# Kernel optimization log

Hardware: AMD Instinct MI355X
Metric: run time of the kernel (lower is better)

## Reference

```python
import jax, jax.numpy as jnp
import numpy as np

B, NQ, NK, D, H, DR, MLPD = 32, 32, 4096, 256, 8, 2, 2048
ID = D // DR  # internal dim for downsampled cross-attention
EPS = 1e-5


def _ln(x, g, b):
    m = jnp.mean(x, -1, keepdims=True)
    v = jnp.mean((x - m) ** 2, -1, keepdims=True)
    return (x - m) / jnp.sqrt(v + EPS) * g + b


def _attn(q, k, v, qw, qb, kw, kb, vw, vb, ow, ob):
    # linear projections (weights stored as [in, out])
    q = q @ qw + qb
    k = k @ kw + kb
    v = v @ vw + vb
    b, nq, c = q.shape
    d = c // H
    qh = q.reshape(b, nq, H, d)
    kh = k.reshape(b, -1, H, d)
    vh = v.reshape(b, -1, H, d)
    scores = jnp.einsum('bqhd,bkhd->bhqk', qh, kh) * (1.0 / np.sqrt(d))
    a = jax.nn.softmax(scores, axis=-1)
    o = jnp.einsum('bhqk,bkhd->bqhd', a, vh).reshape(b, nq, c)
    return o @ ow + ob


def _forward(queries, keys, query_pe,
             sa_qw, sa_qb, sa_kw, sa_kb, sa_vw, sa_vb, sa_ow, sa_ob,
             t2i_qw, t2i_qb, t2i_kw, t2i_kb, t2i_vw, t2i_vb, t2i_ow, t2i_ob,
             i2t_qw, i2t_qb, i2t_kw, i2t_kb, i2t_vw, i2t_vb, i2t_ow, i2t_ob,
             mlp_w1, mlp_b1, mlp_w2, mlp_b2,
             ln1_g, ln1_b, ln2_g, ln2_b, ln3_g, ln3_b, ln4_g, ln4_b):
    # skip_first_layer_pe = False
    queries = queries + query_pe
    attn_out = _attn(queries, queries, queries,
                     sa_qw, sa_qb, sa_kw, sa_kb, sa_vw, sa_vb, sa_ow, sa_ob)
    queries = _ln(queries + attn_out, ln1_g, ln1_b)
    # cross attention: tokens -> image
    q = queries + query_pe
    attn_out = _attn(q, keys, keys,
                     t2i_qw, t2i_qb, t2i_kw, t2i_kb, t2i_vw, t2i_vb, t2i_ow, t2i_ob)
    queries = _ln(queries + attn_out, ln2_g, ln2_b)
    # MLP block (num_layers=1): act(x W1 + b1) W2 + b2, act = ReLU
    mlp_out = jax.nn.relu(queries @ mlp_w1 + mlp_b1) @ mlp_w2 + mlp_b2
    queries = _ln(queries + mlp_out, ln3_g, ln3_b)
    # cross attention: image -> tokens
    q = queries + query_pe
    attn_out = _attn(keys, q, queries,
                     i2t_qw, i2t_qb, i2t_kw, i2t_kb, i2t_vw, i2t_vb, i2t_ow, i2t_ob)
    keys = _ln(keys + attn_out, ln4_g, ln4_b)
    return queries, keys


def setup_inputs() -> dict:
    key = jax.random.key(0)
    ks = iter(jax.random.split(key, 64))
    def w(shape, s=0.02):
        return jax.random.normal(next(ks), shape, jnp.float32) * s
    inp = {
        'queries': w((B, NQ, D), 1.0),
        'keys': w((B, NK, D), 1.0),
        'query_pe': w((B, NQ, D), 1.0),
    }
    for pre, idim in [('sa', D), ('t2i', ID), ('i2t', ID)]:
        inp[pre + '_qw'] = w((D, idim)); inp[pre + '_qb'] = jnp.zeros((idim,), jnp.float32)
        inp[pre + '_kw'] = w((D, idim)); inp[pre + '_kb'] = jnp.zeros((idim,), jnp.float32)
        inp[pre + '_vw'] = w((D, idim)); inp[pre + '_vb'] = jnp.zeros((idim,), jnp.float32)
        inp[pre + '_ow'] = w((idim, D)); inp[pre + '_ob'] = jnp.zeros((D,), jnp.float32)
    inp['mlp_w1'] = w((D, MLPD)); inp['mlp_b1'] = jnp.zeros((MLPD,), jnp.float32)
    inp['mlp_w2'] = w((MLPD, D)); inp['mlp_b2'] = jnp.zeros((D,), jnp.float32)
    for i in range(1, 5):
        inp['ln%d_g' % i] = jnp.ones((D,), jnp.float32)
        inp['ln%d_b' % i] = jnp.zeros((D,), jnp.float32)
    return inp


def reference(queries, keys, query_pe,
              sa_qw, sa_qb, sa_kw, sa_kb, sa_vw, sa_vb, sa_ow, sa_ob,
              t2i_qw, t2i_qb, t2i_kw, t2i_kb, t2i_vw, t2i_vb, t2i_ow, t2i_ob,
              i2t_qw, i2t_qb, i2t_kw, i2t_kb, i2t_vw, i2t_vb, i2t_ow, i2t_ob,
              mlp_w1, mlp_b1, mlp_w2, mlp_b2,
              ln1_g, ln1_b, ln2_g, ln2_b, ln3_g, ln3_b, ln4_g, ln4_b):
    return _forward(queries, keys, query_pe,
                    sa_qw, sa_qb, sa_kw, sa_kb, sa_vw, sa_vb, sa_ow, sa_ob,
                    t2i_qw, t2i_qb, t2i_kw, t2i_kb, t2i_vw, t2i_vb, t2i_ow, t2i_ob,
                    i2t_qw, i2t_qb, i2t_kw, i2t_kb, i2t_vw, i2t_vb, i2t_ow, i2t_ob,
                    mlp_w1, mlp_b1, mlp_w2, mlp_b2,
                    ln1_g, ln1_b, ln2_g, ln2_b, ln3_g, ln3_b, ln4_g, ln4_b)
```

## Files before the change

kernel.cpp:

```cpp
#include <hip/hip_runtime.h>

typedef unsigned short u16;
typedef __attribute__((ext_vector_type(8))) short s16x8;
typedef __attribute__((ext_vector_type(4))) float f32x4;
typedef __attribute__((ext_vector_type(8))) unsigned short u16x8;

__device__ __forceinline__ float b2f(u16 u) {
  union { unsigned int i; float f; } v; v.i = ((unsigned int)u) << 16; return v.f;
}
__device__ __forceinline__ u16 f2b(float f) {
  union { float f; unsigned int i; } v; v.f = f;
  unsigned int r = v.i + 0x7FFFu + ((v.i >> 16) & 1u);
  return (u16)(r >> 16);
}
__device__ __forceinline__ int pk2(float a, float b) {
  return (int)f2b(a) | ((int)f2b(b) << 16);
}

template<bool RELU>
__global__ void __launch_bounds__(256) k_gemm(
    const u16* __restrict__ A, const u16* __restrict__ Wt,
    const float* __restrict__ bias, u16* __restrict__ C, int N, int K)
{
  __shared__ int4 smem4[2048];
  char* AsB = (char*)smem4;
  char* WsB = (char*)smem4 + 16384;
  const int t = threadIdx.x;
  const int lane = t & 63, wid = t >> 6;
  const int wm = wid >> 1, wn = wid & 1;
  const int l16 = lane & 15, lhi = lane >> 4;
  const int bCol = blockIdx.x * 128;
  const int bRow = blockIdx.y * 128;

  f32x4 acc[4][4];
#pragma unroll
  for (int i = 0; i < 4; ++i)
#pragma unroll
    for (int j = 0; j < 4; ++j) acc[i][j] = (f32x4){0.f, 0.f, 0.f, 0.f};

  int4 av[4], wv[4];
  auto LOADT = [&](int kt) {
    const int k0 = kt << 6;
#pragma unroll
    for (int i = 0; i < 4; ++i) {
      int L = i * 4096 + t * 16;
      int r = L >> 7, cl = (L >> 4) & 7;
      av[i] = *(const int4*)(A + (size_t)(bRow + r) * K + k0 + cl * 8);
      wv[i] = *(const int4*)(Wt + (size_t)(bCol + r) * K + k0 + cl * 8);
    }
  };
  const int nk = K >> 6;
  LOADT(0);
  for (int kt = 0; kt < nk; ++kt) {
    if (kt) __syncthreads();
#pragma unroll
    for (int i = 0; i < 4; ++i) {
      int L = i * 4096 + t * 16;
      int r = L >> 7, cl = (L >> 4) & 7;
      int off = r * 128 + ((cl ^ (r & 7)) << 4);
      *(int4*)(AsB + off) = av[i];
      *(int4*)(WsB + off) = wv[i];
    }
    __syncthreads();
    if (kt + 1 < nk) LOADT(kt + 1);
#pragma unroll
    for (int kk = 0; kk < 2; ++kk) {
      s16x8 af[4], bfr[4];
#pragma unroll
      for (int mt = 0; mt < 4; ++mt) {
        int r = wm * 64 + mt * 16 + l16;
        int ch = kk * 4 + lhi;
        af[mt] = *(const s16x8*)(AsB + r * 128 + ((ch ^ (r & 7)) << 4));
      }
#pragma unroll
      for (int nt = 0; nt < 4; ++nt) {
        int r = wn * 64 + nt * 16 + l16;
        int ch = kk * 4 + lhi;
        bfr[nt] = *(const s16x8*)(WsB + r * 128 + ((ch ^ (r & 7)) << 4));
      }
#pragma unroll
      for (int mt = 0; mt < 4; ++mt)
#pragma unroll
        for (int nt = 0; nt < 4; ++nt)
          acc[mt][nt] = __builtin_amdgcn_mfma_f32_16x16x32_bf16(
              af[mt], bfr[nt], acc[mt][nt], 0, 0, 0);
    }
  }
#pragma unroll
  for (int mt = 0; mt < 4; ++mt) {
#pragma unroll
    for (int nt = 0; nt < 4; ++nt) {
      int cg = bCol + wn * 64 + nt * 16 + l16;
      float bv = bias[cg];
#pragma unroll
      for (int rg = 0; rg < 4; ++rg) {
        int rgl = bRow + wm * 64 + mt * 16 + lhi * 4 + rg;
        float v = acc[mt][nt][rg] + bv;
        if (RELU) v = fmaxf(v, 0.f);
        C[(size_t)rgl * N + cg] = f2b(v);
      }
    }
  }
}

__global__ void __launch_bounds__(512, 2) k_gemm_kvq(
    const float* __restrict__ A, const u16* __restrict__ Wt,
    const float* __restrict__ bias, u16* __restrict__ KV, u16* __restrict__ QB)
{
  __shared__ char smem[65536];
  char* AsB = smem;
  char* WsB = smem + 16384;
  const int t = threadIdx.x;
  const int lane = t & 63, wid = t >> 6;
  const int wm = wid >> 2, wn = wid & 3;
  const int l16 = lane & 15, lhi = lane >> 4;
  const int bRow = blockIdx.x * 128;

  f32x4 acc[4][6];
#pragma unroll
  for (int i = 0; i < 4; ++i)
#pragma unroll
    for (int j = 0; j < 6; ++j) acc[i][j] = (f32x4){0.f, 0.f, 0.f, 0.f};

  float4 a0r[2], a1r[2];
  int4 wv[6];
  auto LOADT = [&](int kt) {
    const int k0 = kt << 6;
#pragma unroll
    for (int i = 0; i < 2; ++i) {
      int L = i * 8192 + t * 16;
      int r = L >> 7, cl = (L >> 4) & 7;
      const float* Af = A + (size_t)(bRow + r) * 256 + k0 + cl * 8;
      a0r[i] = *(const float4*)Af;
      a1r[i] = *(const float4*)(Af + 4);
    }
#pragma unroll
    for (int i = 0; i < 6; ++i) {
      int L = i * 8192 + t * 16;
      int r = L >> 7, cl = (L >> 4) & 7;
      wv[i] = *(const int4*)(Wt + (size_t)r * 256 + k0 + cl * 8);
    }
  };
  LOADT(0);
  for (int kt = 0; kt < 4; ++kt) {
    if (kt) __syncthreads();
#pragma unroll
    for (int i = 0; i < 2; ++i) {
      int L = i * 8192 + t * 16;
      int r = L >> 7, cl = (L >> 4) & 7;
      int4 p = (int4){pk2(a0r[i].x, a0r[i].y), pk2(a0r[i].z, a0r[i].w),
                      pk2(a1r[i].x, a1r[i].y), pk2(a1r[i].z, a1r[i].w)};
      *(int4*)(AsB + r * 128 + ((cl ^ (r & 7)) << 4)) = p;
    }
#pragma unroll
    for (int i = 0; i < 6; ++i) {
      int L = i * 8192 + t * 16;
      int r = L >> 7, cl = (L >> 4) & 7;
      *(int4*)(WsB + r * 128 + ((cl ^ (r & 7)) << 4)) = wv[i];
    }
    __syncthreads();
    if (kt < 3) LOADT(kt + 1);
#pragma unroll
    for (int kk = 0; kk < 2; ++kk) {
      s16x8 af[4], bfr[6];
#pragma unroll
      for (int mt = 0; mt < 4; ++mt) {
        int r = wm * 64 + mt * 16 + l16;
        int ch = kk * 4 + lhi;
        af[mt] = *(const s16x8*)(AsB + r * 128 + ((ch ^ (r & 7)) << 4));
      }
#pragma unroll
      for (int nt = 0; nt < 6; ++nt) {
        int r = wn * 96 + nt * 16 + l16;
        int ch = kk * 4 + lhi;
        bfr[nt] = *(const s16x8*)(WsB + r * 128 + ((ch ^ (r & 7)) << 4));
      }
#pragma unroll
      for (int mt = 0; mt < 4; ++mt)
#pragma unroll
        for (int nt = 0; nt < 6; ++nt)
          acc[mt][nt] = __builtin_amdgcn_mfma_f32_16x16x32_bf16(
              af[mt], bfr[nt], acc[mt][nt], 0, 0, 0);
    }
  }
  u16* ldsO = (u16*)smem;
  for (int half = 0; half < 2; ++half) {
    __syncthreads();
    if (wm == half) {
#pragma unroll
      for (int mt = 0; mt < 4; ++mt) {
#pragma unroll
        for (int nt = 0; nt < 6; ++nt) {
          int cg = wn * 96 + nt * 16 + l16;
          float bv = bias[cg];
#pragma unroll
          for (int rg = 0; rg < 4; ++rg) {
            int r = mt * 16 + lhi * 4 + rg;
            ldsO[r * 384 + cg] = f2b(acc[mt][nt][rg] + bv);
          }
        }
      }
    }
    __syncthreads();
#pragma unroll
    for (int i = 0; i < 6; ++i) {
      int chunk = i * 512 + t;
      int r = chunk / 48, c8 = chunk - r * 48;
      int row = bRow + half * 64 + r;
      int4 v = *(int4*)(ldsO + r * 384 + c8 * 8);
      if (c8 < 32) *(int4*)(KV + (size_t)row * 256 + c8 * 8) = v;
      else         *(int4*)(QB + (size_t)row * 128 + (c8 - 32) * 8) = v;
    }
  }
}

__global__ void __launch_bounds__(256) k_gemm_ln(
    const u16* __restrict__ A, const u16* __restrict__ Wt,
    const float* __restrict__ bias, const float* __restrict__ res,
    const float* __restrict__ g, const float* __restrict__ bl,
    float* __restrict__ out)
{
  __shared__ int4 smem4[2560];
  __shared__ float rsum[2][32][2], rsq[2][32][2];
  char* AsB = (char*)smem4;
  char* WsB = (char*)smem4 + 8192;
  const int t = threadIdx.x;
  const int lane = t & 63, wid = t >> 6;
  const int wm = wid >> 1, wn = wid & 1;
  const int l16 = lane & 15, lhi = lane >> 4;
  const int bRow = blockIdx.x * 64;

  f32x4 acc[2][8];
#pragma unroll
  for (int i = 0; i < 2; ++i)
#pragma unroll
    for (int j = 0; j < 8; ++j) acc[i][j] = (f32x4){0.f, 0.f, 0.f, 0.f};

  int4 av[2], wv[8];
  auto LOADT = [&](int kt) {
    const int k0 = kt << 6;
#pragma unroll
    for (int i = 0; i < 2; ++i) {
      int L = i * 4096 + t * 16;
      int r = L >> 7, cl = (L >> 4) & 7;
      av[i] = *(const int4*)(A + (size_t)(bRow + r) * 128 + k0 + cl * 8);
    }
#pragma unroll
    for (int i = 0; i < 8; ++i) {
      int L = i * 4096 + t * 16;
      int r = L >> 7, cl = (L >> 4) & 7;
      wv[i] = *(const int4*)(Wt + (size_t)r * 128 + k0 + cl * 8);
    }
  };
  LOADT(0);
  for (int kt = 0; kt < 2; ++kt) {
    if (kt) __syncthreads();
#pragma unroll
    for (int i = 0; i < 2; ++i) {
      int L = i * 4096 + t * 16;
      int r = L >> 7, cl = (L >> 4) & 7;
      *(int4*)(AsB + r * 128 + ((cl ^ (r & 7)) << 4)) = av[i];
    }
#pragma unroll
    for (int i = 0; i < 8; ++i) {
      int L = i * 4096 + t * 16;
      int r = L >> 7, cl = (L >> 4) & 7;
      *(int4*)(WsB + r * 128 + ((cl ^ (r & 7)) << 4)) = wv[i];
    }
    __syncthreads();
    if (kt == 0) LOADT(1);
#pragma unroll
    for (int kk = 0; kk < 2; ++kk) {
      s16x8 af[2], bfr[8];
#pragma unroll
      for (int mt = 0; mt < 2; ++mt) {
        int r = wm * 32 + mt * 16 + l16;
        int ch = kk * 4 + lhi;
        af[mt] = *(const s16x8*)(AsB + r * 128 + ((ch ^ (r & 7)) << 4));
      }
#pragma unroll
      for (int nt = 0; nt < 8; ++nt) {
        int r = wn * 128 + nt * 16 + l16;
        int ch = kk * 4 + lhi;
        bfr[nt] = *(const s16x8*)(WsB + r * 128 + ((ch ^ (r & 7)) << 4));
      }
#pragma unroll
      for (int mt = 0; mt < 2; ++mt)
#pragma unroll
        for (int nt = 0; nt < 8; ++nt)
          acc[mt][nt] = __builtin_amdgcn_mfma_f32_16x16x32_bf16(
              af[mt], bfr[nt], acc[mt][nt], 0, 0, 0);
    }
  }
#pragma unroll
  for (int mt = 0; mt < 2; ++mt) {
#pragma unroll
    for (int nt = 0; nt < 8; ++nt) {
      int cg = wn * 128 + nt * 16 + l16;
      float bv = bias[cg];
#pragma unroll
      for (int rg = 0; rg < 4; ++rg) {
        int row = bRow + wm * 32 + mt * 16 + lhi * 4 + rg;
        acc[mt][nt][rg] += bv + res[(size_t)row * 256 + cg];
      }
    }
  }
#pragma unroll
  for (int mt = 0; mt < 2; ++mt) {
#pragma unroll
    for (int rg = 0; rg < 4; ++rg) {
      float ps = 0.f, pq = 0.f;
#pragma unroll
      for (int nt = 0; nt < 8; ++nt) {
        float v = acc[mt][nt][rg];
        ps += v; pq += v * v;
      }
#pragma unroll
      for (int msk = 1; msk < 16; msk <<= 1) {
        ps += __shfl_xor(ps, msk);
        pq += __shfl_xor(pq, msk);
      }
      if (l16 == 0) {
        int rl = mt * 16 + lhi * 4 + rg;
        rsum[wm][rl][wn] = ps;
        rsq[wm][rl][wn] = pq;
      }
    }
  }
  __syncthreads();
#pragma unroll
  for (int mt = 0; mt < 2; ++mt) {
#pragma unroll
    for (int rg = 0; rg < 4; ++rg) {
      int rl = mt * 16 + lhi * 4 + rg;
      float ts = rsum[wm][rl][0] + rsum[wm][rl][1];
      float tq = rsq[wm][rl][0] + rsq[wm][rl][1];
      float mean = ts * (1.f / 256.f);
      float var = tq * (1.f / 256.f) - mean * mean;
      float rstd = rsqrtf(var + 1e-5f);
      int row = bRow + wm * 32 + rl;
#pragma unroll
      for (int nt = 0; nt < 8; ++nt) {
        int cg = wn * 128 + nt * 16 + l16;
        out[(size_t)row * 256 + cg] =
            (acc[mt][nt][rg] - mean) * rstd * g[cg] + bl[cg];
      }
    }
  }
}

struct TDesc { const float* src; void* dst; int K; int N; int mode; int blk0; };
struct TArgs { TDesc d[24]; int n; };

__global__ void __launch_bounds__(256) k_trans(TArgs a)
{
  int blk = blockIdx.x;
  int i = 0;
  while (i + 1 < a.n && blk >= a.d[i + 1].blk0) ++i;
  TDesc td = a.d[i];
  int e = (blk - td.blk0) * 256 + threadIdx.x;
  int tot = td.K * td.N;
  if (e >= tot) return;
  if (td.mode == 0) {
    int k = e / td.N, n = e - k * td.N;
    ((u16*)td.dst)[(size_t)n * td.K + k] = f2b(td.src[e]);
  } else {
    ((float*)td.dst)[e] = td.src[e];
  }
}

__global__ void __launch_bounds__(256) k_addpe(
    const float* __restrict__ q, const float* __restrict__ pe,
    float* __restrict__ outf, u16* __restrict__ outb)
{
  int i = blockIdx.x * 256 + threadIdx.x;
  float v = q[i] + pe[i];
  outf[i] = v;
  outb[i] = f2b(v);
}

__global__ void __launch_bounds__(64) k_attn_sa(
    const u16* __restrict__ QKV, u16* __restrict__ out)
{
  __shared__ float Q[32][33], K[32][33], V[32][33];
  int b = blockIdx.x >> 3, h = blockIdx.x & 7;
  int t = threadIdx.x;
  for (int idx = t; idx < 1024; idx += 64) {
    int i = idx >> 5, d = idx & 31;
    size_t base = (size_t)(b * 32 + i) * 768 + h * 32 + d;
    Q[i][d] = b2f(QKV[base]);
    K[i][d] = b2f(QKV[base + 256]);
    V[i][d] = b2f(QKV[base + 512]);
  }
  __syncthreads();
  int i = t & 31, half = t >> 5;
  float s[16];
#pragma unroll
  for (int jj = 0; jj < 16; ++jj) {
    int j = half * 16 + jj;
    float a = 0.f;
#pragma unroll
    for (int d = 0; d < 32; ++d) a += Q[i][d] * K[j][d];
    s[jj] = a * 0.17677669529663687f;
  }
  float m = s[0];
#pragma unroll
  for (int jj = 1; jj < 16; ++jj) m = fmaxf(m, s[jj]);
  m = fmaxf(m, __shfl_xor(m, 32));
  float sum = 0.f;
#pragma unroll
  for (int jj = 0; jj < 16; ++jj) { s[jj] = __expf(s[jj] - m); sum += s[jj]; }
  sum += __shfl_xor(sum, 32);
  float o[32];
#pragma unroll
  for (int d = 0; d < 32; ++d) o[d] = 0.f;
#pragma unroll
  for (int jj = 0; jj < 16; ++jj) {
    int j = half * 16 + jj;
    float p = s[jj];
#pragma unroll
    for (int d = 0; d < 32; ++d) o[d] += p * V[j][d];
  }
  float inv = 1.f / sum;
#pragma unroll
  for (int d = 0; d < 32; ++d) {
    float v = o[d] + __shfl_xor(o[d], 32);
    if (half == 0) out[(size_t)(b * 32 + i) * 256 + h * 32 + d] = f2b(v * inv);
  }
}

__global__ void __launch_bounds__(128) k_attn_t2i_part(
    const u16* __restrict__ Qt, const u16* __restrict__ KV,
    float* __restrict__ part)
{
  __shared__ int4 kvs[4096];
  int c = blockIdx.x, b = blockIdx.y;
  int tid = threadIdx.x;
  const int4* src = (const int4*)(KV + ((size_t)b * 4096 + c * 128) * 256);
  for (int i = tid; i < 4096; i += 128) kvs[i] = src[i];
  __syncthreads();
  int qp = tid >> 3, h = tid & 7;
  const u16* lds = (const u16*)kvs;

  float q0[16], q1[16];
  {
    const u16* p0 = Qt + (size_t)(b * 32 + qp) * 128 + h * 16;
    const u16* p1 = Qt + (size_t)(b * 32 + qp + 16) * 128 + h * 16;
    u16x8 a0 = *(const u16x8*)p0, b0 = *(const u16x8*)(p0 + 8);
    u16x8 a1 = *(const u16x8*)p1, b1 = *(const u16x8*)(p1 + 8);
#pragma unroll
    for (int e = 0; e < 8; ++e) {
      q0[e] = b2f(a0[e]); q0[8 + e] = b2f(b0[e]);
      q1[e] = b2f(a1[e]); q1[8 + e] = b2f(b1[e]);
    }
  }
  float m0 = -INFINITY, s0 = 0.f, m1 = -INFINITY, s1 = 0.f;
  float acc0[16], acc1[16];
#pragma unroll
  for (int d = 0; d < 16; ++d) { acc0[d] = 0.f; acc1[d] = 0.f; }

  for (int j = 0; j < 128; ++j) {
    const u16* kr = lds + j * 256 + h * 16;
    u16x8 ka = *(const u16x8*)kr;
    u16x8 kb = *(const u16x8*)(kr + 8);
    float l0 = 0.f, l1 = 0.f;
#pragma unroll
    for (int e = 0; e < 8; ++e) {
      float klo = b2f(ka[e]), khi = b2f(kb[e]);
      l0 += q0[e] * klo + q0[8 + e] * khi;
      l1 += q1[e] * klo + q1[8 + e] * khi;
    }
    l0 *= 0.25f; l1 *= 0.25f;
    const u16* vr = kr + 128;
    u16x8 va = *(const u16x8*)vr;
    u16x8 vb = *(const u16x8*)(vr + 8);
    float nm0 = fmaxf(m0, l0), nm1 = fmaxf(m1, l1);
    float c0 = __expf(m0 - nm0), p0 = __expf(l0 - nm0);
    float c1 = __expf(m1 - nm1), p1 = __expf(l1 - nm1);
    s0 = s0 * c0 + p0; s1 = s1 * c1 + p1;
#pragma unroll
    for (int e = 0; e < 8; ++e) {
      float vlo = b2f(va[e]), vhi = b2f(vb[e]);
      acc0[e] = acc0[e] * c0 + p0 * vlo;
      acc0[8 + e] = acc0[8 + e] * c0 + p0 * vhi;
      acc1[e] = acc1[e] * c1 + p1 * vlo;
      acc1[8 + e] = acc1[8 + e] * c1 + p1 * vhi;
    }
    m0 = nm0; m1 = nm1;
  }
  float* r0 = part + (((size_t)(b * 32 + qp) * 8 + h) * 32 + c) * 18;
  float* r1 = part + (((size_t)(b * 32 + qp + 16) * 8 + h) * 32 + c) * 18;
#pragma unroll
  for (int d = 0; d < 16; ++d) { r0[d] = acc0[d]; r1[d] = acc1[d]; }
  r0[16] = m0; r0[17] = s0;
  r1[16] = m1; r1[17] = s1;
}

__global__ void __launch_bounds__(256) k_attn_t2i_merge(
    const float* __restrict__ part, u16* __restrict__ out)
{
  int b = blockIdx.x >> 3, h = blockIdx.x & 7;
  int q = threadIdx.x >> 3, ds = threadIdx.x & 7;
  const float* base = part + (((size_t)(b * 32 + q) * 8 + h) * 32) * 18;
  float mg = -INFINITY;
#pragma unroll 4
  for (int c = 0; c < 32; ++c) mg = fmaxf(mg, base[c * 18 + 16]);
  float sg = 0.f, a0 = 0.f, a1 = 0.f;
#pragma unroll 4
  for (int c = 0; c < 32; ++c) {
    const float* rec = base + c * 18;
    float w = __expf(rec[16] - mg);
    sg += rec[17] * w;
    a0 += rec[ds * 2] * w;
    a1 += rec[ds * 2 + 1] * w;
  }
  float inv = 1.f / sg;
  u16* op = out + (size_t)(b * 32 + q) * 128 + h * 16 + ds * 2;
  op[0] = f2b(a0 * inv);
  op[1] = f2b(a1 * inv);
}

__global__ void __launch_bounds__(256) k_attn_i2t(
    const u16* __restrict__ Qb, const u16* __restrict__ Kc,
    const u16* __restrict__ Vc, u16* __restrict__ out)
{
  __shared__ float Kl[32][132], Vl[32][132];
  int blk = blockIdx.x;
  int b = blk >> 7;
  int r0 = (blk & 127) * 32;
  for (int idx = threadIdx.x; idx < 4096; idx += 256) {
    int j = idx >> 7, c = idx & 127;
    Kl[j][c] = b2f(Kc[(size_t)(b * 32 + j) * 128 + c]);
    Vl[j][c] = b2f(Vc[(size_t)(b * 32 + j) * 128 + c]);
  }
  __syncthreads();
  int lr = threadIdx.x >> 3, h = threadIdx.x & 7;
  size_t row = (size_t)b * 4096 + r0 + lr;
  const u16* qp = Qb + row * 128 + h * 16;
  float q[16];
  {
    u16x8 qa = *(const u16x8*)qp;
    u16x8 qb2 = *(const u16x8*)(qp + 8);
#pragma unroll
    for (int e = 0; e < 8; ++e) { q[e] = b2f(qa[e]); q[8 + e] = b2f(qb2[e]); }
  }
  float lg[32];
  float mx = -INFINITY;
#pragma unroll
  for (int j = 0; j < 32; ++j) {
    float a = 0.f;
#pragma unroll
    for (int d = 0; d < 16; ++d) a += q[d] * Kl[j][h * 16 + d];
    lg[j] = a * 0.25f;
    mx = fmaxf(mx, lg[j]);
  }
  float sum = 0.f;
#pragma unroll
  for (int j = 0; j < 32; ++j) { lg[j] = __expf(lg[j] - mx); sum += lg[j]; }
  float acc[16];
#pragma unroll
  for (int d = 0; d < 16; ++d) acc[d] = 0.f;
#pragma unroll
  for (int j = 0; j < 32; ++j) {
    float p = lg[j];
#pragma unroll
    for (int d = 0; d < 16; ++d) acc[d] += p * Vl[j][h * 16 + d];
  }
  float inv = 1.f / sum;
  u16* op = out + row * 128 + h * 16;
#pragma unroll
  for (int d = 0; d < 16; ++d) op[d] = f2b(acc[d] * inv);
}

__global__ void __launch_bounds__(256) k_addln_small(
    const float* __restrict__ res, const u16* __restrict__ delta,
    const float* __restrict__ g, const float* __restrict__ bb,
    float* outf, u16* outb, const float* pe, u16* outpe)
{
  int row = blockIdx.x * 4 + (threadIdx.x >> 6);
  int lane = threadIdx.x & 63;
  size_t base = (size_t)row * 256 + lane * 4;
  float4 xv = *(const float4*)(res + base);
  ushort4 dv = *(const ushort4*)(delta + base);
  float v0 = xv.x + b2f(dv.x), v1 = xv.y + b2f(dv.y);
  float v2 = xv.z + b2f(dv.z), v3 = xv.w + b2f(dv.w);
  float sum = v0 + v1 + v2 + v3;
  float sq = v0 * v0 + v1 * v1 + v2 * v2 + v3 * v3;
#pragma unroll
  for (int msk = 1; msk < 64; msk <<= 1) {
    sum += __shfl_xor(sum, msk);
    sq += __shfl_xor(sq, msk);
  }
  float mean = sum * (1.f / 256.f);
  float var = sq * (1.f / 256.f) - mean * mean;
  float rstd = rsqrtf(var + 1e-5f);
  float4 gv = *(const float4*)(g + lane * 4);
  float4 bv = *(const float4*)(bb + lane * 4);
  float y0 = (v0 - mean) * rstd * gv.x + bv.x;
  float y1 = (v1 - mean) * rstd * gv.y + bv.y;
  float y2 = (v2 - mean) * rstd * gv.z + bv.z;
  float y3 = (v3 - mean) * rstd * gv.w + bv.w;
  if (outf) { float4 o{y0, y1, y2, y3}; *(float4*)(outf + base) = o; }
  if (outb) {
    ushort4 o{f2b(y0), f2b(y1), f2b(y2), f2b(y3)};
    *(ushort4*)(outb + base) = o;
  }
  if (outpe) {
    float4 pv = *(const float4*)(pe + base);
    ushort4 o{f2b(y0 + pv.x), f2b(y1 + pv.y), f2b(y2 + pv.z), f2b(y3 + pv.w)};
    *(ushort4*)(outpe + base) = o;
  }
}

extern "C" void kernel_launch(void* const* d_in, const int* in_sizes, int n_in,
                              void* d_out, int out_size, void* d_ws, size_t ws_size,
                              hipStream_t stream)
{
  (void)in_sizes; (void)n_in; (void)out_size; (void)ws_size;
  const float* queries = (const float*)d_in[0];
  const float* keys    = (const float*)d_in[1];
  const float* qpe     = (const float*)d_in[2];
  const float* sa_qw = (const float*)d_in[3];  const float* sa_qb = (const float*)d_in[4];
  const float* sa_kw = (const float*)d_in[5];  const float* sa_kb = (const float*)d_in[6];
  const float* sa_vw = (const float*)d_in[7];  const float* sa_vb = (const float*)d_in[8];
  const float* sa_ow = (const float*)d_in[9];  const float* sa_ob = (const float*)d_in[10];
  const float* t2i_qw = (const float*)d_in[11]; const float* t2i_qb = (const float*)d_in[12];
  const float* t2i_kw = (const float*)d_in[13]; const float* t2i_kb = (const float*)d_in[14];
  const float* t2i_vw = (const float*)d_in[15]; const float* t2i_vb = (const float*)d_in[16];
  const float* t2i_ow = (const float*)d_in[17]; const float* t2i_ob = (const float*)d_in[18];
  const float* i2t_qw = (const float*)d_in[19]; const float* i2t_qb = (const float*)d_in[20];
  const float* i2t_kw = (const float*)d_in[21]; const float* i2t_kb = (const float*)d_in[22];
  const float* i2t_vw = (const float*)d_in[23]; const float* i2t_vb = (const float*)d_in[24];
  const float* i2t_ow = (const float*)d_in[25]; const float* i2t_ob = (const float*)d_in[26];
  const float* mlp_w1 = (const float*)d_in[27]; const float* mlp_b1 = (const float*)d_in[28];
  const float* mlp_w2 = (const float*)d_in[29]; const float* mlp_b2 = (const float*)d_in[30];
  const float* ln1_g = (const float*)d_in[31]; const float* ln1_b = (const float*)d_in[32];
  const float* ln2_g = (const float*)d_in[33]; const float* ln2_b = (const float*)d_in[34];
  const float* ln3_g = (const float*)d_in[35]; const float* ln3_b = (const float*)d_in[36];
  const float* ln4_g = (const float*)d_in[37]; const float* ln4_b = (const float*)d_in[38];

  float* out_q = (float*)d_out;
  float* out_k = out_q + 262144;

  u16* kvbuf  = (u16*)out_k;
  u16* qb_big = (u16*)out_k + 33554432;
  float* t2i_part = (float*)((u16*)out_k + 50331648);

  char* ws = (char*)d_ws;
  size_t off = 0;
  auto alloc = [&](size_t bytes) -> char* {
    char* p = ws + off;
    off += (bytes + 255) & ~(size_t)255;
    return p;
  };
  u16* wt_saqkv = (u16*)alloc(768 * 256 * 2);
  u16* wt_saow  = (u16*)alloc(256 * 256 * 2);
  u16* wt_t2iq  = (u16*)alloc(128 * 256 * 2);
  u16* wt_kvq   = (u16*)alloc(384 * 256 * 2);
  u16* wt_t2io  = (u16*)alloc(256 * 128 * 2);
  u16* wt_i2tk  = (u16*)alloc(128 * 256 * 2);
  u16* wt_i2tv  = (u16*)alloc(128 * 256 * 2);
  u16* wt_i2to  = (u16*)alloc(256 * 128 * 2);
  u16* wt_w1    = (u16*)alloc(2048 * 256 * 2);
  u16* wt_w2    = (u16*)alloc(256 * 2048 * 2);
  float* b_saqkv = (float*)alloc(768 * 4);
  float* b_kvq   = (float*)alloc(384 * 4);
  float* q0f = (float*)alloc(262144 * 4);
  float* q1f = (float*)alloc(262144 * 4);
  float* q2f = (float*)alloc(262144 * 4);
  u16* q0b   = (u16*)alloc(262144 * 2);
  u16* qkvs  = (u16*)alloc(786432 * 2);
  u16* attn1 = (u16*)alloc(262144 * 2);
  u16* o1    = (u16*)alloc(262144 * 2);
  u16* q1pe  = (u16*)alloc(262144 * 2);
  u16* qt    = (u16*)alloc(131072 * 2);
  u16* at2   = (u16*)alloc(131072 * 2);
  u16* o2    = (u16*)alloc(262144 * 2);
  u16* q2b   = (u16*)alloc(262144 * 2);
  u16* hbuf  = (u16*)alloc(2097152 * 2);
  u16* mo    = (u16*)alloc(262144 * 2);
  u16* q3b   = (u16*)alloc(262144 * 2);
  u16* q3pe  = (u16*)alloc(262144 * 2);
  u16* kc    = (u16*)alloc(131072 * 2);
  u16* vc    = (u16*)alloc(131072 * 2);
  u16* ab_big = (u16*)alloc((size_t)16777216 * 2);

  TArgs ta{};
  int nb = 0, id = 0;
  auto addT = [&](const float* s, void* d, int K, int N, int mode) {
    ta.d[id].src = s; ta.d[id].dst = d; ta.d[id].K = K; ta.d[id].N = N;
    ta.d[id].mode = mode; ta.d[id].blk0 = nb;
    nb += (K * N + 255) / 256;
    ++id;
  };
  addT(sa_qw, wt_saqkv, 256, 256, 0);
  addT(sa_kw, wt_saqkv + 256 * 256, 256, 256, 0);
  addT(sa_vw, wt_saqkv + 512 * 256, 256, 256, 0);
  addT(sa_ow, wt_saow, 256, 256, 0);
  addT(t2i_qw, wt_t2iq, 256, 128, 0);
  addT(t2i_kw, wt_kvq, 256, 128, 0);
  addT(t2i_vw, wt_kvq + 128 * 256, 256, 128, 0);
  addT(i2t_qw, wt_kvq + 256 * 256, 256, 128, 0);
  addT(t2i_ow, wt_t2io, 128, 256, 0);
  addT(i2t_kw, wt_i2tk, 256, 128, 0);
  addT(i2t_vw, wt_i2tv, 256, 128, 0);
  addT(i2t_ow, wt_i2to, 128, 256, 0);
  addT(mlp_w1, wt_w1, 256, 2048, 0);
  addT(mlp_w2, wt_w2, 2048, 256, 0);
  addT(sa_qb, b_saqkv, 1, 256, 1);
  addT(sa_kb, b_saqkv + 256, 1, 256, 1);
  addT(sa_vb, b_saqkv + 512, 1, 256, 1);
  addT(t2i_kb, b_kvq, 1, 128, 1);
  addT(t2i_vb, b_kvq + 128, 1, 128, 1);
  addT(i2t_qb, b_kvq + 256, 1, 128, 1);
  ta.n = id;
  k_trans<<<nb, 256, 0, stream>>>(ta);

  k_addpe<<<1024, 256, 0, stream>>>(queries, qpe, q0f, q0b);
  k_gemm<false><<<dim3(6, 8), 256, 0, stream>>>(q0b, wt_saqkv, b_saqkv,
                                                qkvs, 768, 256);
  k_attn_sa<<<256, 64, 0, stream>>>(qkvs, attn1);
  k_gemm<false><<<dim3(2, 8), 256, 0, stream>>>(attn1, wt_saow, sa_ob,
                                                o1, 256, 256);
  k_addln_small<<<256, 256, 0, stream>>>(q0f, o1, ln1_g, ln1_b, q1f, nullptr,
                                         qpe, q1pe);
  k_gemm<false><<<dim3(1, 8), 256, 0, stream>>>(q1pe, wt_t2iq, t2i_qb,
                                                qt, 128, 256);
  k_gemm_kvq<<<1024, 512, 0, stream>>>(keys, wt_kvq, b_kvq, kvbuf, qb_big);
  k_attn_t2i_part<<<dim3(32, 32), 128, 0, stream>>>(qt, kvbuf, t2i_part);
  k_attn_t2i_merge<<<256, 256, 0, stream>>>(t2i_part, at2);
  k_gemm<false><<<dim3(2, 8), 256, 0, stream>>>(at2, wt_t2io, t2i_ob,
                                                o2, 256, 128);
  k_addln_small<<<256, 256, 0, stream>>>(q1f, o2, ln2_g, ln2_b, q2f, q2b,
                                         nullptr, nullptr);
  k_gemm<true><<<dim3(16, 8), 256, 0, stream>>>(q2b, wt_w1, mlp_b1,
                                                hbuf, 2048, 256);
  k_gemm<false><<<dim3(2, 8), 256, 0, stream>>>(hbuf, wt_w2, mlp_b2,
                                                mo, 256, 2048);
  k_addln_small<<<256, 256, 0, stream>>>(q2f, mo, ln3_g, ln3_b, out_q, q3b,
                                         qpe, q3pe);
  k_gemm<false><<<dim3(1, 8), 256, 0, stream>>>(q3pe, wt_i2tk, i2t_kb,
                                                kc, 128, 256);
  k_gemm<false><<<dim3(1, 8), 256, 0, stream>>>(q3b, wt_i2tv, i2t_vb,
                                                vc, 128, 256);
  k_attn_i2t<<<4096, 256, 0, stream>>>(qb_big, kc, vc, ab_big);
  k_gemm_ln<<<2048, 256, 0, stream>>>(ab_big, wt_i2to, i2t_ob, keys,
                                      ln4_g, ln4_b, out_k);
}
```

Measured before the change: 609.0 us.

## Fuse t2i attention into KVQ projection and GEMM+LayerNorm for query path

The key/value/query projection kernel now keeps the projected K/V tile in shared memory and runs the token-to-image partial attention directly from it. This removes the round trip of the large KV buffer through global memory and one kernel launch. Separately, the three small output-projection GEMMs are fused with residual-add plus LayerNorm into a new k_gemm_lnq kernel, dropping intermediate buffers and launches. The trade-offs are that the fused kernel uses more LDS (80KB), which may lower occupancy, only half its threads do the attention tail, and the LN GEMMs run on just 16 blocks.

After: 642.3 us. 1.05x slower.

```diff
diff --git a/kernel.cpp b/kernel.cpp
--- a/kernel.cpp
+++ b/kernel.cpp
@@ -103,11 +103,12 @@
   }
 }
 
-__global__ void __launch_bounds__(512, 2) k_gemm_kvq(
+__global__ void __launch_bounds__(512, 2) k_kvq_t2i(
     const float* __restrict__ A, const u16* __restrict__ Wt,
-    const float* __restrict__ bias, u16* __restrict__ KV, u16* __restrict__ QB)
-{
-  __shared__ char smem[65536];
+    const float* __restrict__ bias, const u16* __restrict__ Qt,
+    u16* __restrict__ QB, float* __restrict__ part)
+{
+  __shared__ char smem[81920];
   char* AsB = smem;
   char* WsB = smem + 16384;
   const int t = threadIdx.x;
@@ -183,7 +184,8 @@
               af[mt], bfr[nt], acc[mt][nt], 0, 0, 0);
     }
   }
-  u16* ldsO = (u16*)smem;
+  u16* ldsKV = (u16*)smem;
+  u16* ldsQB = (u16*)(smem + 65536);
   for (int half = 0; half < 2; ++half) {
     __syncthreads();
     if (wm == half) {
@@ -196,20 +198,200 @@
 #pragma unroll
           for (int rg = 0; rg < 4; ++rg) {
             int r = mt * 16 + lhi * 4 + rg;
-            ldsO[r * 384 + cg] = f2b(acc[mt][nt][rg] + bv);
+            u16 o = f2b(acc[mt][nt][rg] + bv);
+            if (cg < 256) ldsKV[(half * 64 + r) * 256 + cg] = o;
+            else          ldsQB[r * 128 + (cg - 256)] = o;
           }
         }
       }
     }
     __syncthreads();
 #pragma unroll
-    for (int i = 0; i < 6; ++i) {
+    for (int i = 0; i < 2; ++i) {
       int chunk = i * 512 + t;
-      int r = chunk / 48, c8 = chunk - r * 48;
-      int row = bRow + half * 64 + r;
-      int4 v = *(int4*)(ldsO + r * 384 + c8 * 8);
-      if (c8 < 32) *(int4*)(KV + (size_t)row * 256 + c8 * 8) = v;
-      else         *(int4*)(QB + (size_t)row * 128 + (c8 - 32) * 8) = v;
+      int r = chunk >> 4, c8 = chunk & 15;
+      *(int4*)(QB + (size_t)(bRow + half * 64 + r) * 128 + c8 * 8) =
+          *(int4*)(ldsQB + r * 128 + c8 * 8);
+    }
+  }
+  if (t < 256) {
+    int q = t >> 3, h = t & 7;
+    int b = bRow >> 12, c = (bRow >> 7) & 31;
+    float q16[16];
+    {
+      const u16* qp = Qt + (size_t)(b * 32 + q) * 128 + h * 16;
+      u16x8 qa = *(const u16x8*)qp;
+      u16x8 qb = *(const u16x8*)(qp + 8);
+#pragma unroll
+      for (int e = 0; e < 8; ++e) { q16[e] = b2f(qa[e]); q16[8 + e] = b2f(qb[e]); }
+    }
+    float m = -INFINITY, s = 0.f, a16[16];
+#pragma unroll
+    for (int d = 0; d < 16; ++d) a16[d] = 0.f;
+    for (int j = 0; j < 128; ++j) {
+      const u16* kr = ldsKV + j * 256 + h * 16;
+      u16x8 ka = *(const u16x8*)kr;
+      u16x8 kb = *(const u16x8*)(kr + 8);
+      float lg = 0.f;
+#pragma unroll
+      for (int e = 0; e < 8; ++e) lg += q16[e] * b2f(ka[e]) + q16[8 + e] * b2f(kb[e]);
+      lg *= 0.25f;
+      const u16* vr = ldsKV + j * 256 + 128 + h * 16;
+      u16x8 va = *(const u16x8*)vr;
+      u16x8 vb = *(const u16x8*)(vr + 8);
+      float nm = fmaxf(m, lg);
+      float corr = __expf(m - nm), p = __expf(lg - nm);
+      s = s * corr + p;
+#pragma unroll
+      for (int e = 0; e < 8; ++e) {
+        a16[e] = a16[e] * corr + p * b2f(va[e]);
+        a16[8 + e] = a16[8 + e] * corr + p * b2f(vb[e]);
+      }
+      m = nm;
+    }
+    float* rec = part + (((size_t)(b * 32 + q) * 8 + h) * 32 + c) * 18;
+#pragma unroll
+    for (int d = 0; d < 16; ++d) rec[d] = a16[d];
+    rec[16] = m; rec[17] = s;
+  }
+}
+
+__global__ void __launch_bounds__(256) k_gemm_lnq(
+    const u16* __restrict__ A, const u16* __restrict__ Wt,
+    const float* __restrict__ bias, const float* __restrict__ res,
+    const float* __restrict__ g, const float* __restrict__ bl,
+    const float* __restrict__ pe,
+    float* outf, u16* outb, u16* outpe, int K)
+{
+  __shared__ int4 smem4[2560];
+  __shared__ float rsum[2][32][2], rsq[2][32][2];
+  char* AsB = (char*)smem4;
+  char* WsB = (char*)smem4 + 8192;
+  const int t = threadIdx.x;
+  const int lane = t & 63, wid = t >> 6;
+  const int wm = wid >> 1, wn = wid & 1;
+  const int l16 = lane & 15, lhi = lane >> 4;
+  const int bRow = blockIdx.x * 64;
+
+  f32x4 acc[2][8];
+#pragma unroll
+  for (int i = 0; i < 2; ++i)
+#pragma unroll
+    for (int j = 0; j < 8; ++j) acc[i][j] = (f32x4){0.f, 0.f, 0.f, 0.f};
+
+  int4 av[2], wv[8];
+  auto LOADT = [&](int kt) {
+    const int k0 = kt << 6;
+#pragma unroll
+    for (int i = 0; i < 2; ++i) {
+      int L = i * 4096 + t * 16;
+      int r = L >> 7, cl = (L >> 4) & 7;
+      av[i] = *(const int4*)(A + (size_t)(bRow + r) * K + k0 + cl * 8);
+    }
+#pragma unroll
+    for (int i = 0; i < 8; ++i) {
+      int L = i * 4096 + t * 16;
+      int r = L >> 7, cl = (L >> 4) & 7;
+      wv[i] = *(const int4*)(Wt + (size_t)r * K + k0 + cl * 8);
+    }
+  };
+  const int nk = K >> 6;
+  LOADT(0);
+  for (int kt = 0; kt < nk; ++kt) {
+    if (kt) __syncthreads();
+#pragma unroll
+    for (int i = 0; i < 2; ++i) {
+      int L = i * 4096 + t * 16;
+      int r = L >> 7, cl = (L >> 4) & 7;
+      *(int4*)(AsB + r * 128 + ((cl ^ (r & 7)) << 4)) = av[i];
+    }
+#pragma unroll
+    for (int i = 0; i < 8; ++i) {
+      int L = i * 4096 + t * 16;
+      int r = L >> 7, cl = (L >> 4) & 7;
+      *(int4*)(WsB + r * 128 + ((cl ^ (r & 7)) << 4)) = wv[i];
+    }
+    __syncthreads();
+    if (kt + 1 < nk) LOADT(kt + 1);
+#pragma unroll
+    for (int kk = 0; kk < 2; ++kk) {
+      s16x8 af[2], bfr[8];
+#pragma unroll
+      for (int mt = 0; mt < 2; ++mt) {
+        int r = wm * 32 + mt * 16 + l16;
+        int ch = kk * 4 + lhi;
+        af[mt] = *(const s16x8*)(AsB + r * 128 + ((ch ^ (r & 7)) << 4));
+      }
+#pragma unroll
+      for (int nt = 0; nt < 8; ++nt) {
+        int r = wn * 128 + nt * 16 + l16;
+        int ch = kk * 4 + lhi;
+        bfr[nt] = *(const s16x8*)(WsB + r * 128 + ((ch ^ (r & 7)) << 4));
+      }
+#pragma unroll
+      for (int mt = 0; mt < 2; ++mt)
+#pragma unroll
+        for (int nt = 0; nt < 8; ++nt)
+          acc[mt][nt] = __builtin_amdgcn_mfma_f32_16x16x32_bf16(
+              af[mt], bfr[nt], acc[mt][nt], 0, 0, 0);
+    }
+  }
+#pragma unroll
+  for (int mt = 0; mt < 2; ++mt) {
+#pragma unroll
+    for (int nt = 0; nt < 8; ++nt) {
+      int cg = wn * 128 + nt * 16 + l16;
+      float bv = bias[cg];
+#pragma unroll
+      for (int rg = 0; rg < 4; ++rg) {
+        int row = bRow + wm * 32 + mt * 16 + lhi * 4 + rg;
+        acc[mt][nt][rg] += bv + res[(size_t)row * 256 + cg];
+      }
+    }
+  }
+#pragma unroll
+  for (int mt = 0; mt < 2; ++mt) {
+#pragma unroll
+    for (int rg = 0; rg < 4; ++rg) {
+      float ps = 0.f, pq = 0.f;
+#pragma unroll
+      for (int nt = 0; nt < 8; ++nt) {
+        float v = acc[mt][nt][rg];
+        ps += v; pq += v * v;
+      }
+#pragma unroll
+      for (int msk = 1; msk < 16; msk <<= 1) {
+        ps += __shfl_xor(ps, msk);
+        pq += __shfl_xor(pq, msk);
+      }
+      if (l16 == 0) {
+        int rl = mt * 16 + lhi * 4 + rg;
+        rsum[wm][rl][wn] = ps;
+        rsq[wm][rl][wn] = pq;
+      }
+    }
+  }
+  __syncthreads();
+#pragma unroll
+  for (int mt = 0; mt < 2; ++mt) {
+#pragma unroll
+    for (int rg = 0; rg < 4; ++rg) {
+      int rl = mt * 16 + lhi * 4 + rg;
+      float ts = rsum[wm][rl][0] + rsum[wm][rl][1];
+      float tq = rsq[wm][rl][0] + rsq[wm][rl][1];
+      float mean = ts * (1.f / 256.f);
+      float var = tq * (1.f / 256.f) - mean * mean;
+      float rstd = rsqrtf(var + 1e-5f);
+      int row = bRow + wm * 32 + rl;
+#pragma unroll
+      for (int nt = 0; nt < 8; ++nt) {
+        int cg = wn * 128 + nt * 16 + l16;
+        size_t idx = (size_t)row * 256 + cg;
+        float y = (acc[mt][nt][rg] - mean) * rstd * g[cg] + bl[cg];
+        if (outf) outf[idx] = y;
+        if (outb) outb[idx] = f2b(y);
+        if (outpe) outpe[idx] = f2b(y + pe[idx]);
+      }
     }
   }
 }
@@ -427,73 +609,6 @@
     float v = o[d] + __shfl_xor(o[d], 32);
     if (half == 0) out[(size_t)(b * 32 + i) * 256 + h * 32 + d] = f2b(v * inv);
   }
-}
-
-__global__ void __launch_bounds__(128) k_attn_t2i_part(
-    const u16* __restrict__ Qt, const u16* __restrict__ KV,
-    float* __restrict__ part)
-{
-  __shared__ int4 kvs[4096];
-  int c = blockIdx.x, b = blockIdx.y;
-  int tid = threadIdx.x;
-  const int4* src = (const int4*)(KV + ((size_t)b * 4096 + c * 128) * 256);
-  for (int i = tid; i < 4096; i += 128) kvs[i] = src[i];
-  __syncthreads();
-  int qp = tid >> 3, h = tid & 7;
-  const u16* lds = (const u16*)kvs;
-
-  float q0[16], q1[16];
-  {
-    const u16* p0 = Qt + (size_t)(b * 32 + qp) * 128 + h * 16;
-    const u16* p1 = Qt + (size_t)(b * 32 + qp + 16) * 128 + h * 16;
-    u16x8 a0 = *(const u16x8*)p0, b0 = *(const u16x8*)(p0 + 8);
-    u16x8 a1 = *(const u16x8*)p1, b1 = *(const u16x8*)(p1 + 8);
-#pragma unroll
-    for (int e = 0; e < 8; ++e) {
-      q0[e] = b2f(a0[e]); q0[8 + e] = b2f(b0[e]);
-      q1[e] = b2f(a1[e]); q1[8 + e] = b2f(b1[e]);
-    }
-  }
-  float m0 = -INFINITY, s0 = 0.f, m1 = -INFINITY, s1 = 0.f;
-  float acc0[16], acc1[16];
-#pragma unroll
-  for (int d = 0; d < 16; ++d) { acc0[d] = 0.f; acc1[d] = 0.f; }
-
-  for (int j = 0; j < 128; ++j) {
-    const u16* kr = lds + j * 256 + h * 16;
-    u16x8 ka = *(const u16x8*)kr;
-    u16x8 kb = *(const u16x8*)(kr + 8);
-    float l0 = 0.f, l1 = 0.f;
-#pragma unroll
-    for (int e = 0; e < 8; ++e) {
-      float klo = b2f(ka[e]), khi = b2f(kb[e]);
-      l0 += q0[e] * klo + q0[8 + e] * khi;
-      l1 += q1[e] * klo + q1[8 + e] * khi;
-    }
-    l0 *= 0.25f; l1 *= 0.25f;
-    const u16* vr = kr + 128;
-    u16x8 va = *(const u16x8*)vr;
-    u16x8 vb = *(const u16x8*)(vr + 8);
-    float nm0 = fmaxf(m0, l0), nm1 = fmaxf(m1, l1);
-    float c0 = __expf(m0 - nm0), p0 = __expf(l0 - nm0);
-    float c1 = __expf(m1 - nm1), p1 = __expf(l1 - nm1);
-    s0 = s0 * c0 + p0; s1 = s1 * c1 + p1;
-#pragma unroll
-    for (int e = 0; e < 8; ++e) {
-      float vlo = b2f(va[e]), vhi = b2f(vb[e]);
-      acc0[e] = acc0[e] * c0 + p0 * vlo;
-      acc0[8 + e] = acc0[8 + e] * c0 + p0 * vhi;
-      acc1[e] = acc1[e] * c1 + p1 * vlo;
-      acc1[8 + e] = acc1[8 + e] * c1 + p1 * vhi;
-    }
-    m0 = nm0; m1 = nm1;
-  }
-  float* r0 = part + (((size_t)(b * 32 + qp) * 8 + h) * 32 + c) * 18;
-  float* r1 = part + (((size_t)(b * 32 + qp + 16) * 8 + h) * 32 + c) * 18;
-#pragma unroll
-  for (int d = 0; d < 16; ++d) { r0[d] = acc0[d]; r1[d] = acc1[d]; }
-  r0[16] = m0; r0[17] = s0;
-  r1[16] = m1; r1[17] = s1;
 }
 
 __global__ void __launch_bounds__(256) k_attn_t2i_merge(
@@ -570,46 +685,6 @@
   u16* op = out + row * 128 + h * 16;
 #pragma unroll
   for (int d = 0; d < 16; ++d) op[d] = f2b(acc[d] * inv);
-}
-
-__global__ void __launch_bounds__(256) k_addln_small(
-    const float* __restrict__ res, const u16* __restrict__ delta,
-    const float* __restrict__ g, const float* __restrict__ bb,
-    float* outf, u16* outb, const float* pe, u16* outpe)
-{
-  int row = blockIdx.x * 4 + (threadIdx.x >> 6);
-  int lane = threadIdx.x & 63;
-  size_t base = (size_t)row * 256 + lane * 4;
-  float4 xv = *(const float4*)(res + base);
-  ushort4 dv = *(const ushort4*)(delta + base);
-  float v0 = xv.x + b2f(dv.x), v1 = xv.y + b2f(dv.y);
-  float v2 = xv.z + b2f(dv.z), v3 = xv.w + b2f(dv.w);
-  float sum = v0 + v1 + v2 + v3;
-  float sq = v0 * v0 + v1 * v1 + v2 * v2 + v3 * v3;
-#pragma unroll
-  for (int msk = 1; msk < 64; msk <<= 1) {
-    sum += __shfl_xor(sum, msk);
-    sq += __shfl_xor(sq, msk);
-  }
-  float mean = sum * (1.f / 256.f);
-  float var = sq * (1.f / 256.f) - mean * mean;
-  float rstd = rsqrtf(var + 1e-5f);
-  float4 gv = *(const float4*)(g + lane * 4);
-  float4 bv = *(const float4*)(bb + lane * 4);
-  float y0 = (v0 - mean) * rstd * gv.x + bv.x;
-  float y1 = (v1 - mean) * rstd * gv.y + bv.y;
-  float y2 = (v2 - mean) * rstd * gv.z + bv.z;
-  float y3 = (v3 - mean) * rstd * gv.w + bv.w;
-  if (outf) { float4 o{y0, y1, y2, y3}; *(float4*)(outf + base) = o; }
-  if (outb) {
-    ushort4 o{f2b(y0), f2b(y1), f2b(y2), f2b(y3)};
-    *(ushort4*)(outb + base) = o;
-  }
-  if (outpe) {
-    float4 pv = *(const float4*)(pe + base);
-    ushort4 o{f2b(y0 + pv.x), f2b(y1 + pv.y), f2b(y2 + pv.z), f2b(y3 + pv.w)};
-    *(ushort4*)(outpe + base) = o;
-  }
 }
 
 extern "C" void kernel_launch(void* const* d_in, const int* in_sizes, int n_in,
@@ -642,7 +717,6 @@
   float* out_q = (float*)d_out;
   float* out_k = out_q + 262144;
 
-  u16* kvbuf  = (u16*)out_k;
   u16* qb_big = (u16*)out_k + 33554432;
   float* t2i_part = (float*)((u16*)out_k + 50331648);
 
@@ -671,14 +745,11 @@
   u16* q0b   = (u16*)alloc(262144 * 2);
   u16* qkvs  = (u16*)alloc(786432 * 2);
   u16* attn1 = (u16*)alloc(262144 * 2);
-  u16* o1    = (u16*)alloc(262144 * 2);
   u16* q1pe  = (u16*)alloc(262144 * 2);
   u16* qt    = (u16*)alloc(131072 * 2);
   u16* at2   = (u16*)alloc(131072 * 2);
-  u16* o2    = (u16*)alloc(262144 * 2);
   u16* q2b   = (u16*)alloc(262144 * 2);
   u16* hbuf  = (u16*)alloc(2097152 * 2);
-  u16* mo    = (u16*)alloc(262144 * 2);
   u16* q3b   = (u16*)alloc(262144 * 2);
   u16* q3pe  = (u16*)alloc(262144 * 2);
   u16* kc    = (u16*)alloc(131072 * 2);
@@ -720,25 +791,22 @@
   k_gemm<false><<<dim3(6, 8), 256, 0, stream>>>(q0b, wt_saqkv, b_saqkv,
                                                 qkvs, 768, 256);
   k_attn_sa<<<256, 64, 0, stream>>>(qkvs, attn1);
-  k_gemm<false><<<dim3(2, 8), 256, 0, stream>>>(attn1, wt_saow, sa_ob,
-                                                o1, 256, 256);
-  k_addln_small<<<256, 256, 0, stream>>>(q0f, o1, ln1_g, ln1_b, q1f, nullptr,
-                                         qpe, q1pe);
+  k_gemm_lnq<<<16, 256, 0, stream>>>(attn1, wt_saow, sa_ob, q0f,
+                                     ln1_g, ln1_b, qpe,
+                                     q1f, nullptr, q1pe, 256);
   k_gemm<false><<<dim3(1, 8), 256, 0, stream>>>(q1pe, wt_t2iq, t2i_qb,
                                                 qt, 128, 256);
-  k_gemm_kvq<<<1024, 512, 0, stream>>>(keys, wt_kvq, b_kvq, kvbuf, qb_big);
-  k_attn_t2i_part<<<dim3(32, 32), 128, 0, stream>>>(qt, kvbuf, t2i_part);
+  k_kvq_t2i<<<1024, 512, 0, stream>>>(keys, wt_kvq, b_kvq, qt, qb_big,
+                                      t2i_part);
   k_attn_t2i_merge<<<256, 256, 0, stream>>>(t2i_part, at2);
-  k_gemm<false><<<dim3(2, 8), 256, 0, stream>>>(at2, wt_t2io, t2i_ob,
-                                                o2, 256, 128);
-  k_addln_small<<<256, 256, 0, stream>>>(q1f, o2, ln2_g, ln2_b, q2f, q2b,
-                                         nullptr, nullptr);
+  k_gemm_lnq<<<16, 256, 0, stream>>>(at2, wt_t2io, t2i_ob, q1f,
+                                     ln2_g, ln2_b, nullptr,
+                                     q2f, q2b, nullptr, 128);
   k_gemm<true><<<dim3(16, 8), 256, 0, stream>>>(q2b, wt_w1, mlp_b1,
                                                 hbuf, 2048, 256);
-  k_gemm<false><<<dim3(2, 8), 256, 0, stream>>>(hbuf, wt_w2, mlp_b2,
-                                                mo, 256, 2048);
-  k_addln_small<<<256, 256, 0, stream>>>(q2f, mo, ln3_g, ln3_b, out_q, q3b,
-                                         qpe, q3pe);
+  k_gemm_lnq<<<16, 256, 0, stream>>>(hbuf, wt_w2, mlp_b2, q2f,
+                                     ln3_g, ln3_b, qpe,
+                                     out_q, q3b, q3pe, 2048);
   k_gemm<false><<<dim3(1, 8), 256, 0, stream>>>(q3pe, wt_i2tk, i2t_kb,
                                                 kc, 128, 256);
   k_gemm<false><<<dim3(1, 8), 256, 0, stream>>>(q3b, wt_i2tv, i2t_vb,
```
